# Optimization experiments

Hardware: AMD Instinct MI355X
Metric: run time of the kernel (lower is better)

## Reference

```python
import jax, jax.numpy as jnp
import numpy as np

N_NODES, N_EDGES = 10000, 100000
NODE_DIM, NUM_BASIS = 128, 20
MULS = {0: 128, 1: 64, 2: 32}            # 128x0e + 64x1e + 32x2e
NUM_IRREPS = 224                          # total multiplicity count
HIDDEN = NODE_DIM + NUM_IRREPS            # 352
SPH_DIM = 128 * 1 + 64 * 3 + 32 * 5       # 480
LN_EPS = 1e-5

def _s2_basis():
    # orthonormal (Frobenius) basis of symmetric traceless 3x3 matrices (real l=2)
    s = np.zeros((5, 3, 3)); r2 = 1.0 / np.sqrt(2.0)
    s[0, 0, 1] = s[0, 1, 0] = r2
    s[1, 1, 2] = s[1, 2, 1] = r2
    s[2] = np.diag([-1.0, -1.0, 2.0]) / np.sqrt(6.0)
    s[3, 0, 2] = s[3, 2, 0] = r2
    s[4] = np.diag([1.0, -1.0, 0.0]) * r2
    return s

def _cg_tables():
    # real Clebsch-Gordan tensors for l<=2 built from the invariant tensors
    # delta, Levi-Civita, and the symmetric-traceless basis; unit Frobenius norm (e3nn w3j convention)
    e3 = np.zeros((3, 3, 3))
    e3[0, 1, 2] = e3[1, 2, 0] = e3[2, 0, 1] = 1.0
    e3[0, 2, 1] = e3[2, 1, 0] = e3[1, 0, 2] = -1.0
    S = _s2_basis(); I3 = np.eye(3); I5 = np.eye(5)
    nrm = lambda c: (c / np.linalg.norm(c)).astype(np.float32)
    cg = {(0, 0, 0): np.ones((1, 1, 1), np.float32)}
    cg[(0, 1, 1)] = nrm(I3[None]); cg[(1, 0, 1)] = nrm(I3[:, None, :]); cg[(1, 1, 0)] = nrm(I3[:, :, None])
    cg[(0, 2, 2)] = nrm(I5[None]); cg[(2, 0, 2)] = nrm(I5[:, None, :]); cg[(2, 2, 0)] = nrm(I5[:, :, None])
    cg[(1, 1, 1)] = nrm(e3)
    cg[(1, 1, 2)] = nrm(np.transpose(S, (1, 2, 0)))
    cg[(1, 2, 1)] = nrm(np.transpose(S, (1, 0, 2)))
    cg[(2, 1, 1)] = nrm(S)
    cg[(2, 2, 1)] = nrm(np.einsum('ijk,Mil,Nlj->MNk', e3, S, S))
    cg[(1, 2, 2)] = nrm(np.einsum('iab,Mac,Ncb->iMN', e3, S, S))
    cg[(2, 1, 2)] = nrm(np.einsum('jab,Mac,Ncb->MjN', e3, S, S))
    cg[(2, 2, 2)] = nrm(np.einsum('Mab,Nbc,Pca->MNP', S, S, S))
    return cg

CG = _cg_tables()
PATHS = [(0, 0, 0), (1, 1, 0), (2, 2, 0),
         (0, 1, 1), (1, 0, 1), (1, 1, 1), (1, 2, 1), (2, 1, 1), (2, 2, 1),
         (0, 2, 2), (1, 1, 2), (1, 2, 2), (2, 0, 2), (2, 1, 2), (2, 2, 2)]
FAN = {0: 224, 1: 384, 2: 352}   # e3nn 'element' path-norm fan-in per output irrep
TP_NUMW = sum(MULS[l1] * MULS[l3] for (l1, _, l3) in PATHS)

def _layernorm(x, w, b):
    mu = x.mean(-1, keepdims=True)
    var = ((x - mu) ** 2).mean(-1, keepdims=True)
    return (x - mu) * jax.lax.rsqrt(var + LN_EPS) * w + b

def _o3_layernorm(x, w, b):
    # equivariant layer norm: per-irrep RMS over (mul, m); mean-centering + bias only for scalars
    n = x.shape[0]; outs = []; off = 0; woff = 0
    for l in (0, 1, 2):
        mul, d = MULS[l], 2 * l + 1
        f = x[:, off:off + mul * d].reshape(n, mul, d)
        if l == 0:
            f = f - f.mean(axis=1, keepdims=True)
        nrm = (f * f).mean(axis=(1, 2), keepdims=True)
        f = f * jax.lax.rsqrt(nrm + LN_EPS) * w[woff:woff + mul][None, :, None]
        if l == 0:
            f = f + b[None, :, None]
        outs.append(f.reshape(n, mul * d)); off += mul * d; woff += mul
    return jnp.concatenate(outs, -1)

def _fc_tp(x1, x2, tp_w):
    # FullyConnectedTensorProduct(128x0e+64x1e+32x2e, 1x0e+1x1e+1x2e -> 128x0e+64x1e+32x2e)
    outs = {0: 0.0, 1: 0.0, 2: 0.0}; off = 0
    for (l1, l2, l3) in PATHS:
        m1, m3 = MULS[l1], MULS[l3]
        W = tp_w[off:off + m1 * m3].reshape(m1, m3); off += m1 * m3
        pw = float(np.sqrt((2 * l3 + 1) / FAN[l3]))
        outs[l3] = outs[l3] + pw * jnp.einsum('eum,en,mnk,uw->ewk', x1[l1], x2[l2], jnp.asarray(CG[(l1, l2, l3)]), W, optimize=True)
    e = x2[0].shape[0]
    return jnp.concatenate([outs[l].reshape(e, -1) for l in (0, 1, 2)], -1)

def _forward(x_scalar, x_spherical, rbf, rsh, ln_w, ln_b, o3_w, o3_b,
             mlp_w1, mlp_b1, mlp_w2, mlp_b2, rbf_w, tp_w, edge_index):
    scalar_in = _layernorm(x_scalar, ln_w, ln_b)                # [N,128]
    spherical_in = _o3_layernorm(x_spherical, o3_w, o3_b)       # [N,480]
    h = jax.nn.silu(scalar_in @ mlp_w1 + mlp_b1)
    scalar_out = h @ mlp_w2 + mlp_b2                            # [N,352]
    filt = rbf @ rbf_w                                          # [E,352]
    dst, src = edge_index[0], edge_index[1]
    fo = scalar_out[src] * filt                                 # gather + RBF filter
    gate, msg_scalar = fo[:, :NUM_IRREPS], fo[:, NUM_IRREPS:]
    sph = spherical_in[src]                                     # [E,480]
    e = sph.shape[0]
    # ElementwiseTensorProduct(edge_irreps, 224x0e): per-channel scalar gating
    x1 = {0: (sph[:, :128] * gate[:, :128])[:, :, None],
          1: sph[:, 128:320].reshape(e, 64, 3) * gate[:, 128:192, None],
          2: sph[:, 320:480].reshape(e, 32, 5) * gate[:, 192:224, None]}
    x2 = {0: rsh[:, :1], 1: rsh[:, 1:4], 2: rsh[:, 4:9]}
    msg_sph = _fc_tp(x1, x2, tp_w)                              # [E,480]
    new_scalar = scalar_in.at[dst].add(msg_scalar)
    new_spherical = spherical_in.at[dst].add(msg_sph)
    return new_scalar, new_spherical

def setup_inputs():
    key = jax.random.key(0)
    ks = jax.random.split(key, 9)
    return {
        'x_scalar': jax.random.normal(ks[0], (N_NODES, NODE_DIM), jnp.float32),
        'x_spherical': jax.random.normal(ks[1], (N_NODES, SPH_DIM), jnp.float32),
        'rbf': jax.random.uniform(ks[2], (N_EDGES, NUM_BASIS), jnp.float32),
        'rsh': jax.random.normal(ks[3], (N_EDGES, 9), jnp.float32),
        'edge_index': jax.random.randint(ks[4], (2, N_EDGES), 0, N_NODES, dtype=jnp.int32),
        'ln_w': jnp.ones((NODE_DIM,), jnp.float32),
        'ln_b': jnp.zeros((NODE_DIM,), jnp.float32),
        'o3_w': jnp.ones((NUM_IRREPS,), jnp.float32),
        'o3_b': jnp.zeros((128,), jnp.float32),
        'mlp_w1': jax.random.normal(ks[5], (NODE_DIM, NODE_DIM), jnp.float32) / np.sqrt(NODE_DIM),
        'mlp_b1': jnp.zeros((NODE_DIM,), jnp.float32),
        'mlp_w2': jax.random.normal(ks[6], (NODE_DIM, HIDDEN), jnp.float32) / np.sqrt(NODE_DIM),
        'mlp_b2': jnp.zeros((HIDDEN,), jnp.float32),
        'rbf_w': jax.random.normal(ks[7], (NUM_BASIS, HIDDEN), jnp.float32) / np.sqrt(NUM_BASIS),
        'tp_w': jax.random.normal(ks[8], (TP_NUMW,), jnp.float32),
    }

def reference(x_scalar, x_spherical, rbf, rsh, edge_index, ln_w, ln_b, o3_w, o3_b,
              mlp_w1, mlp_b1, mlp_w2, mlp_b2, rbf_w, tp_w):
    return _forward(x_scalar, x_spherical, rbf, rsh, ln_w, ln_b, o3_w, o3_b,
                    mlp_w1, mlp_b1, mlp_w2, mlp_b2, rbf_w, tp_w, edge_index)
```

## Files before the change

kernel.cpp:

```cpp
#include <hip/hip_runtime.h>

#define NN 10000
#define NE 100000
#define ND 128
#define NB 20
#define NIR 224
#define NH 352
#define SD 480
#define BS 512

#define CR   0.70710678118654752f
#define CA   0.40824829046386302f
#define HA   0.20412414523193151f
#define HR   0.35355339059327376f
#define C110 0.57735026918962576f
#define C220 0.44721359549995794f
#define C111 0.40824829046386302f
#define C11X 0.44721359549995794f
#define C221 0.36514837167011074f
#define C222 0.58554004376912270f
#define S32  0.86602540378443865f
#define PW0  0.066815310478106094f
#define PW1  0.088388347648318447f
#define PW2  0.11918321088232916f

typedef __bf16 v8bf __attribute__((ext_vector_type(8)));
typedef unsigned short us8v __attribute__((ext_vector_type(8)));
typedef float f32x4 __attribute__((ext_vector_type(4)));

__device__ __forceinline__ unsigned short f2bfc(float f) {
  __bf16 h = (__bf16)f;
  return __builtin_bit_cast(unsigned short, h);
}
__device__ __forceinline__ float bf2f(unsigned short h) {
  unsigned int u = ((unsigned int)h) << 16;
  return __builtin_bit_cast(float, u);
}

__device__ __forceinline__ float warpReduceSum(float v) {
  #pragma unroll
  for (int off = 32; off > 0; off >>= 1) v += __shfl_down(v, off, 64);
  return v;
}

__device__ __forceinline__ int t2tT(int t) {
  if (t < 128) return t;
  if (t < 320) { int c = t - 128; return 128 + (c % 3) * 64 + c / 3; }
  int c = t - 320; return 320 + (c % 5) * 32 + c / 5;
}

__global__ __launch_bounds__(256) void sort_hist(const int* __restrict__ ei, int* __restrict__ cnt) {
  int e = blockIdx.x * 256 + threadIdx.x;
  if (e < NE) atomicAdd(&cnt[ei[e]], 1);
}

__global__ __launch_bounds__(1024) void sort_scan(const int* __restrict__ cnt, int* __restrict__ cursor) {
  __shared__ int part[1024];
  const int t = threadIdx.x;
  int loc[10]; int s = 0;
  #pragma unroll
  for (int j = 0; j < 10; ++j) { int idx = t * 10 + j; int v = (idx < NN) ? cnt[idx] : 0; loc[j] = s; s += v; }
  part[t] = s; __syncthreads();
  for (int d = 1; d < 1024; d <<= 1) {
    int v = (t >= d) ? part[t - d] : 0; __syncthreads();
    part[t] += v; __syncthreads();
  }
  int off = part[t] - s;
  #pragma unroll
  for (int j = 0; j < 10; ++j) { int idx = t * 10 + j; if (idx < NN) cursor[idx] = off + loc[j]; }
}

__global__ __launch_bounds__(256) void sort_scatter(
    const int* __restrict__ ei, int* __restrict__ cursor,
    int* __restrict__ es_eid) {
  int e = blockIdx.x * 256 + threadIdx.x;
  if (e < NE) {
    int d = ei[e];
    int pos = atomicAdd(&cursor[d], 1);
    es_eid[pos] = e;
  }
}

__global__ __launch_bounds__(128) void node_ln_kernel(
    const float* __restrict__ xs, const float* __restrict__ xsph,
    const float* __restrict__ lnw, const float* __restrict__ lnb,
    const float* __restrict__ o3w, const float* __restrict__ o3b,
    float* __restrict__ s_in, float* __restrict__ sphT,
    float* __restrict__ out0)
{
  const int n = blockIdx.x, t = threadIdx.x;
  __shared__ float red[4];

  auto reduce2 = [&](float a, float b) {
    a = warpReduceSum(a); b = warpReduceSum(b);
    if ((t & 63) == 0) { red[(t >> 6) * 2] = a; red[(t >> 6) * 2 + 1] = b; }
    __syncthreads();
    float ra = red[0] + red[2], rb = red[1] + red[3];
    __syncthreads();
    return make_float2(ra, rb);
  };

  float x = xs[n * ND + t];
  float2 sr = reduce2(x, x * x);
  float mu = sr.x * (1.f / ND);
  float var = sr.y * (1.f / ND) - mu * mu;
  float y = (x - mu) * rsqrtf(var + 1e-5f) * lnw[t] + lnb[t];
  s_in[n * ND + t] = y; out0[n * ND + t] = y;

  float f = xsph[n * SD + t];
  float2 r0 = reduce2(f, f * f);
  float m0 = r0.x * (1.f / 128.f);
  float nrm0 = r0.y * (1.f / 128.f) - m0 * m0;
  float y0 = (f - m0) * rsqrtf(nrm0 + 1e-5f) * o3w[t] + o3b[t];
  sphT[n * SD + t] = y0;

  float f1a = xsph[n * SD + 128 + t];
  float f1b = (t < 64) ? xsph[n * SD + 256 + t] : 0.f;
  float2 r1 = reduce2(f1a * f1a + f1b * f1b, 0.f);
  float rs1 = rsqrtf(r1.x * (1.f / 192.f) + 1e-5f);
  sphT[n * SD + t2tT(128 + t)] = f1a * rs1 * o3w[128 + t / 3];
  if (t < 64)
    sphT[n * SD + t2tT(256 + t)] = f1b * rs1 * o3w[128 + (128 + t) / 3];

  float f2a = xsph[n * SD + 320 + t];
  float f2b = (t < 32) ? xsph[n * SD + 448 + t] : 0.f;
  float2 r2 = reduce2(f2a * f2a + f2b * f2b, 0.f);
  float rs2 = rsqrtf(r2.x * (1.f / 160.f) + 1e-5f);
  sphT[n * SD + t2tT(320 + t)] = f2a * rs2 * o3w[192 + t / 5];
  if (t < 32)
    sphT[n * SD + t2tT(448 + t)] = f2b * rs2 * o3w[192 + (128 + t) / 5];
}

#define NPB 8
__global__ __launch_bounds__(256) void mlp_kernel(
    const float* __restrict__ s_in, const float* __restrict__ w1,
    const float* __restrict__ b1, const float* __restrict__ w2,
    const float* __restrict__ b2, float* __restrict__ s_out)
{
  __shared__ float sIn[NPB][ND];
  __shared__ float sH[NPB][ND];
  const int t = threadIdx.x;
  const int n0 = blockIdx.x * NPB;
  for (int i = t; i < NPB * ND; i += 256) sIn[i >> 7][i & 127] = s_in[n0 * ND + i];
  __syncthreads();
  {
    const int j = t & 127, g = t >> 7;
    float acc[4] = {0.f, 0.f, 0.f, 0.f};
    for (int k = 0; k < ND; ++k) {
      float w = w1[k * ND + j];
      #pragma unroll
      for (int i = 0; i < 4; ++i) acc[i] = fmaf(sIn[g + 2 * i][k], w, acc[i]);
    }
    #pragma unroll
    for (int i = 0; i < 4; ++i) {
      float z = acc[i] + b1[j];
      sH[g + 2 * i][j] = z / (1.f + __expf(-z));
    }
  }
  __syncthreads();
  for (int jb = 0; jb < 2; ++jb) {
    int j = jb * 256 + t;
    if (j < NH) {
      float acc[NPB];
      #pragma unroll
      for (int i = 0; i < NPB; ++i) acc[i] = b2[j];
      for (int k = 0; k < ND; ++k) {
        float w = w2[k * NH + j];
        #pragma unroll
        for (int i = 0; i < NPB; ++i) acc[i] = fmaf(sH[i][k], w, acc[i]);
      }
      #pragma unroll
      for (int i = 0; i < NPB; ++i) s_out[(n0 + i) * NH + j] = acc[i];
    }
  }
}

__device__ __forceinline__ float wc0(const float* w, int u, int j) {
  int off = (u < 128) ? u * 128 : (u < 192) ? 16384 + (u - 128) * 128 : 24576 + (u - 192) * 128;
  return w[off + j];
}
__device__ __forceinline__ float wc1(const float* w, int u, int j) {
  int off = (u < 128) ? 28672 + u * 64 : (u < 192) ? 36864 + (u - 128) * 64
          : (u < 256) ? 40960 + (u - 192) * 64 : (u < 320) ? 45056 + (u - 256) * 64
          : (u < 352) ? 49152 + (u - 320) * 64 : 51200 + (u - 352) * 64;
  return w[off + j];
}
__device__ __forceinline__ float wc2(const float* w, int u, int j) {
  int off = (u < 128) ? 53248 + u * 32 : (u < 192) ? 57344 + (u - 128) * 32
          : (u < 256) ? 59392 + (u - 192) * 32 : (u < 288) ? 61440 + (u - 256) * 32
          : (u < 320) ? 62464 + (u - 288) * 32 : 63488 + (u - 320) * 32;
  return w[off + j];
}

__global__ __launch_bounds__(256) void prep_w_kernel(
    const float* __restrict__ tpw, const float* __restrict__ rbf_w,
    unsigned short* __restrict__ W0g, unsigned short* __restrict__ W1g,
    unsigned short* __restrict__ W2g, unsigned short* __restrict__ Wfq)
{
  int gid = blockIdx.x * 256 + threadIdx.x;
  int i = gid & 7, lane = (gid >> 3) & 63;
  int r = lane & 15, kl = lane >> 4;
  if (gid < 28672) {
    int fid = gid >> 9, kk = fid >> 3, wid = fid & 7;
    W0g[gid] = f2bfc(wc0(tpw, kk * 32 + kl * 8 + i, wid * 16 + r));
  } else if (gid < 53248) {
    int g = gid - 28672, fid = g >> 9, kk = fid >> 2, nt = fid & 3;
    W1g[g] = f2bfc(wc1(tpw, kk * 32 + kl * 8 + i, nt * 16 + r));
  } else if (gid < 65536) {
    int g = gid - 53248, fid = g >> 9, q = fid >> 2, kh = (fid >> 1) & 1, ntc = fid & 1;
    int kk = kh * 6 + q;
    W2g[g] = (kk < 11) ? f2bfc(wc2(tpw, kk * 32 + kl * 8 + i, ntc * 16 + r)) : (unsigned short)0;
  } else if (gid < 90112) {
    int g = gid - 65536, fid = g >> 9, q = fid >> 3, wid = fid & 7;
    int t44 = wid + q * 8, nt = t44 >> 1, k = kl * 8 + i;
    Wfq[g] = (t44 < 44 && k < 20) ? f2bfc(rbf_w[k * NH + nt * 16 + r]) : (unsigned short)0;
  }
}

template<int M>
__device__ __forceinline__ void emit_dot(unsigned short* dst, const unsigned short* x1,
                                         const int* offs, const float* cf) {
  us8v xv[M];
  #pragma unroll
  for (int m = 0; m < M; ++m) xv[m] = *(const us8v*)&x1[offs[m]];
  v8bf o;
  #pragma unroll
  for (int i = 0; i < 8; ++i) {
    float a = 0.f;
    #pragma unroll
    for (int m = 0; m < M; ++m) a = fmaf(cf[m], bf2f(xv[m][i]), a);
    o[i] = (__bf16)a;
  }
  *(us8v*)dst = __builtin_bit_cast(us8v, o);
}

#define TSW(e, idx) ((idx) ^ (((e) & 7) << 3))

__device__ __forceinline__ void build0(unsigned short* Tb, const unsigned short* X1u,
                                       const float* RshF, int tid) {
  for (int it = tid; it < 32 * 28; it += BS) {
    int e = it / 28, ub = it - e * 28, u0 = ub * 8;
    const float* R = &RshF[e * 9];
    const unsigned short* x1 = &X1u[e * 480];
    unsigned short* dst = Tb + TSW(e, e * 384 + u0);
    if (u0 < 128) {
      float cf[1] = { PW0 * R[0] };
      int offs[1] = { u0 };
      emit_dot<1>(dst, x1, offs, cf);
    } else if (u0 < 192) {
      int m0 = u0 - 128;
      float cf[3] = { PW0 * C110 * R[1], PW0 * C110 * R[2], PW0 * C110 * R[3] };
      int offs[3] = { 128 + m0, 192 + m0, 256 + m0 };
      emit_dot<3>(dst, x1, offs, cf);
    } else {
      int m0 = u0 - 192;
      float cf[5] = { PW0 * C220 * R[4], PW0 * C220 * R[5], PW0 * C220 * R[6],
                      PW0 * C220 * R[7], PW0 * C220 * R[8] };
      int offs[5] = { 320 + m0, 352 + m0, 384 + m0, 416 + m0, 448 + m0 };
      emit_dot<5>(dst, x1, offs, cf);
    }
  }
}

template<int k>
__device__ __forceinline__ void build1(unsigned short* Tb, const unsigned short* X1u,
                                       const float* RshF, int tid) {
  for (int it = tid; it < 32 * 48; it += BS) {
    int e = it / 48, ub = it - e * 48, u0 = ub * 8;
    const float* R = &RshF[e * 9];
    const unsigned short* x1 = &X1u[e * 480];
    unsigned short* dst = Tb + TSW(e, e * 384 + u0);
    const float s = R[0], v0 = R[1], v1 = R[2], v2 = R[3];
    const float w0 = R[4], w1 = R[5], w2 = R[6], w3 = R[7], w4 = R[8];
    if (u0 < 128) {
      float cf[1] = { PW1 * C110 * R[1 + k] };
      int offs[1] = { u0 };
      emit_dot<1>(dst, x1, offs, cf);
    } else if (u0 < 192) {
      float cf[1] = { PW1 * C110 * s };
      int offs[1] = { 128 + k * 64 + (u0 - 128) };
      emit_dot<1>(dst, x1, offs, cf);
    } else if (u0 < 256) {
      constexpr int ka = (k + 1) % 3, kb = (k + 2) % 3;
      int m0 = u0 - 192;
      float cf[2] = { PW1 * C111 * R[1 + kb], -PW1 * C111 * R[1 + ka] };
      int offs[2] = { 128 + ka * 64 + m0, 128 + kb * 64 + m0 };
      emit_dot<2>(dst, x1, offs, cf);
    } else if (u0 < 320) {
      int m0 = u0 - 256;
      float cf[3];
      if constexpr (k == 0) { cf[0] = PW1*C11X*(-CA*w2 + CR*w4); cf[1] = PW1*C11X*CR*w0; cf[2] = PW1*C11X*CR*w3; }
      else if constexpr (k == 1) { cf[0] = PW1*C11X*CR*w0; cf[1] = PW1*C11X*(-CA*w2 - CR*w4); cf[2] = PW1*C11X*CR*w1; }
      else { cf[0] = PW1*C11X*CR*w3; cf[1] = PW1*C11X*CR*w1; cf[2] = PW1*C11X*2.f*CA*w2; }
      int offs[3] = { 128 + m0, 192 + m0, 256 + m0 };
      emit_dot<3>(dst, x1, offs, cf);
    } else if (u0 < 352) {
      int m0 = u0 - 320;
      if constexpr (k == 0) {
        float cf[4] = { PW1*C11X*CR*v1, PW1*C11X*(-CA*v0), PW1*C11X*CR*v2, PW1*C11X*CR*v0 };
        int offs[4] = { 320 + m0, 384 + m0, 416 + m0, 448 + m0 };
        emit_dot<4>(dst, x1, offs, cf);
      } else if constexpr (k == 1) {
        float cf[4] = { PW1*C11X*CR*v0, PW1*C11X*CR*v2, PW1*C11X*(-CA*v1), PW1*C11X*(-CR*v1) };
        int offs[4] = { 320 + m0, 352 + m0, 384 + m0, 448 + m0 };
        emit_dot<4>(dst, x1, offs, cf);
      } else {
        float cf[3] = { PW1*C11X*CR*v1, PW1*C11X*2.f*CA*v2, PW1*C11X*CR*v0 };
        int offs[3] = { 352 + m0, 384 + m0, 416 + m0 };
        emit_dot<3>(dst, x1, offs, cf);
      }
    } else {
      int m0 = u0 - 352;
      if constexpr (k == 0) {
        float cf[5] = { PW1*C221*0.5f*w3, PW1*C221*(S32*w2 + 0.5f*w4), PW1*C221*(-S32*w1),
                        PW1*C221*(-0.5f*w0), PW1*C221*(-0.5f*w1) };
        int offs[5] = { 320 + m0, 352 + m0, 384 + m0, 416 + m0, 448 + m0 };
        emit_dot<5>(dst, x1, offs, cf);
      } else if constexpr (k == 1) {
        float cf[5] = { PW1*C221*(-0.5f*w1), PW1*C221*0.5f*w0, PW1*C221*S32*w3,
                        PW1*C221*(-S32*w2 + 0.5f*w4), PW1*C221*(-0.5f*w3) };
        int offs[5] = { 320 + m0, 352 + m0, 384 + m0, 416 + m0, 448 + m0 };
        emit_dot<5>(dst, x1, offs, cf);
      } else {
        float cf[4] = { PW1*C221*(-w4), PW1*C221*(-0.5f*w3), PW1*C221*0.5f*w1, PW1*C221*w0 };
        int offs[4] = { 320 + m0, 352 + m0, 416 + m0, 448 + m0 };
        emit_dot<4>(dst, x1, offs, cf);
      }
    }
  }
}

template<int K>
__device__ __forceinline__ void build2(unsigned short* Tb, const unsigned short* X1u,
                                       const float* RshF, int tid) {
  for (int it = tid; it < 32 * 44; it += BS) {
    int e = it / 44, ub = it - e * 44, u0 = ub * 8;
    const float* R = &RshF[e * 9];
    const unsigned short* x1 = &X1u[e * 480];
    unsigned short* dst = Tb + TSW(e, e * 384 + u0);
    const float s = R[0], v0 = R[1], v1 = R[2], v2 = R[3];
    const float w0 = R[4], w1 = R[5], w2 = R[6], w3 = R[7], w4 = R[8];
    if (u0 < 128) {
      float cf[1] = { PW2 * C220 * R[4 + K] };
      int offs[1] = { u0 };
      emit_dot<1>(dst, x1, offs, cf);
    } else if (u0 < 192) {
      int m0 = u0 - 128;
      if constexpr (K == 0) {
        float cf[2] = { PW2*C11X*CR*v1, PW2*C11X*CR*v0 };
        int offs[2] = { 128 + m0, 192 + m0 };
        emit_dot<2>(dst, x1, offs, cf);
      } else if constexpr (K == 1) {
        float cf[2] = { PW2*C11X*CR*v2, PW2*C11X*CR*v1 };
        int offs[2] = { 192 + m0, 256 + m0 };
        emit_dot<2>(dst, x1, offs, cf);
      } else if constexpr (K == 2) {
        float cf[3] = { PW2*C11X*(-CA*v0), PW2*C11X*(-CA*v1), PW2*C11X*2.f*CA*v2 };
        int offs[3] = { 128 + m0, 192 + m0, 256 + m0 };
        emit_dot<3>(dst, x1, offs, cf);
      } else if constexpr (K == 3) {
        float cf[2] = { PW2*C11X*CR*v2, PW2*C11X*CR*v0 };
        int offs[2] = { 128 + m0, 256 + m0 };
        emit_dot<2>(dst, x1, offs, cf);
      } else {
        float cf[2] = { PW2*C11X*CR*v0, PW2*C11X*(-CR*v1) };
        int offs[2] = { 128 + m0, 192 + m0 };
        emit_dot<2>(dst, x1, offs, cf);
      }
    } else if (u0 < 256) {
      int m0 = u0 - 192;
      if constexpr (K == 2) {
        float cf[2] = { PW2*C221*S32*w1, PW2*C221*(-S32*w3) };
        int offs[2] = { 128 + m0, 192 + m0 };
        emit_dot<2>(dst, x1, offs, cf);
      } else {
        float cf[3];
        if constexpr (K == 0) { cf[0]=PW2*C221*(-0.5f*w3); cf[1]=PW2*C221*0.5f*w1; cf[2]=PW2*C221*w4; }
        else if constexpr (K == 1) { cf[0]=PW2*C221*(-S32*w2 - 0.5f*w4); cf[1]=PW2*C221*(-0.5f*w0); cf[2]=PW2*C221*0.5f*w3; }
        else if constexpr (K == 3) { cf[0]=PW2*C221*0.5f*w0; cf[1]=PW2*C221*(S32*w2 - 0.5f*w4); cf[2]=PW2*C221*(-0.5f*w1); }
        else { cf[0]=PW2*C221*0.5f*w1; cf[1]=PW2*C221*0.5f*w3; cf[2]=PW2*C221*(-w0); }
        int offs[3] = { 128 + m0, 192 + m0, 256 + m0 };
        emit_dot<3>(dst, x1, offs, cf);
      }
    } else if (u0 < 288) {
      int m0 = u0 - 256;
      float cf[1] = { PW2 * C220 * s };
      int offs[1] = { 320 + K * 32 + m0 };
      emit_dot<1>(dst, x1, offs, cf);
    } else if (u0 < 320) {
      int m0 = u0 - 288;
      if constexpr (K == 0) {
        float cf[3] = { PW2*C221*0.5f*v1, PW2*C221*(-0.5f*v0), PW2*C221*v2 };
        int offs[3] = { 352 + m0, 416 + m0, 448 + m0 };
        emit_dot<3>(dst, x1, offs, cf);
      } else if constexpr (K == 1) {
        float cf[4] = { PW2*C221*(-0.5f*v1), PW2*C221*(-S32*v0), PW2*C221*0.5f*v2, PW2*C221*(-0.5f*v0) };
        int offs[4] = { 320 + m0, 384 + m0, 416 + m0, 448 + m0 };
        emit_dot<4>(dst, x1, offs, cf);
      } else if constexpr (K == 2) {
        float cf[2] = { PW2*C221*S32*v0, PW2*C221*(-S32*v1) };
        int offs[2] = { 352 + m0, 416 + m0 };
        emit_dot<2>(dst, x1, offs, cf);
      } else if constexpr (K == 3) {
        float cf[4] = { PW2*C221*0.5f*v0, PW2*C221*(-0.5f*v2), PW2*C221*S32*v1, PW2*C221*(-0.5f*v1) };
        int offs[4] = { 320 + m0, 352 + m0, 384 + m0, 448 + m0 };
        emit_dot<4>(dst, x1, offs, cf);
      } else {
        float cf[3] = { PW2*C221*(-v2), PW2*C221*0.5f*v0, PW2*C221*0.5f*v1 };
        int offs[3] = { 320 + m0, 352 + m0, 416 + m0 };
        emit_dot<3>(dst, x1, offs, cf);
      }
    } else {
      int m0 = u0 - 320;
      if constexpr (K == 0) {
        float cf[4] = { PW2*C222*(-CA*w2), PW2*C222*HR*w3, PW2*C222*(-CA*w0), PW2*C222*HR*w1 };
        int offs[4] = { 320 + m0, 352 + m0, 384 + m0, 416 + m0 };
        emit_dot<4>(dst, x1, offs, cf);
      } else if constexpr (K == 4) {
        float cf[4] = { PW2*C222*(-HR*w1), PW2*C222*(-CA*w4), PW2*C222*HR*w3, PW2*C222*(-CA*w2) };
        int offs[4] = { 352 + m0, 384 + m0, 416 + m0, 448 + m0 };
        emit_dot<4>(dst, x1, offs, cf);
      } else {
        float cf[5];
        if constexpr (K == 1) { cf[0]=PW2*C222*HR*w3; cf[1]=PW2*C222*(HA*w2 - HR*w4); cf[2]=PW2*C222*HA*w1; cf[3]=PW2*C222*HR*w0; cf[4]=PW2*C222*(-HR*w1); }
        else if constexpr (K == 2) { cf[0]=PW2*C222*(-CA*w0); cf[1]=PW2*C222*HA*w1; cf[2]=PW2*C222*CA*w2; cf[3]=PW2*C222*HA*w3; cf[4]=PW2*C222*(-CA*w4); }
        else { cf[0]=PW2*C222*HR*w1; cf[1]=PW2*C222*HR*w0; cf[2]=PW2*C222*HA*w3; cf[3]=PW2*C222*(HA*w2 + HR*w4); cf[4]=PW2*C222*HR*w3; }
        int offs[5] = { 320 + m0, 352 + m0, 384 + m0, 416 + m0, 448 + m0 };
        emit_dot<5>(dst, x1, offs, cf);
      }
    }
  }
}

__global__ __launch_bounds__(BS, 4) void tp_fused_kernel(
    const float* __restrict__ rbf, const float* __restrict__ rsh,
    const int* __restrict__ ei, const float* __restrict__ s_out,
    const float* __restrict__ sphT,
    const unsigned short* __restrict__ W0g, const unsigned short* __restrict__ W1g,
    const unsigned short* __restrict__ W2g, const unsigned short* __restrict__ Wfq,
    float* __restrict__ out0, unsigned short* __restrict__ msgT)
{
  __shared__ __align__(16) unsigned char smem[81280];
  unsigned short* Tb0 = (unsigned short*)smem;
  unsigned short* Tb1 = (unsigned short*)(smem + 24576);
  unsigned short* gateU = (unsigned short*)smem;
  unsigned short* rbfpadU = (unsigned short*)(smem + 24576);
  unsigned short* X1u = (unsigned short*)(smem + 49152);
  float* RshF = (float*)(smem + 79872);
  int* EdstS = (int*)(smem + 81024);
  int* EsrcS = (int*)(smem + 81152);

  const int tid = threadIdx.x;
  const int wid = tid >> 6, lane = tid & 63;
  const int r = lane & 15, kl = lane >> 4;

  auto MFMA = [](v8bf a, v8bf b, f32x4 c) {
    return __builtin_amdgcn_mfma_f32_16x16x32_bf16(a, b, c, 0, 0, 0);
  };
  auto ldw = [&](const unsigned short* base, int fid) {
    return __builtin_bit_cast(v8bf, *(const us8v*)&base[fid * 512 + lane * 8]);
  };

  auto mfma_l0 = [&](const unsigned short* T, long ebase) {
    f32x4 acc0 = {0.f, 0.f, 0.f, 0.f}, acc1 = {0.f, 0.f, 0.f, 0.f};
    #pragma unroll
    for (int kk = 0; kk < 7; ++kk) {
      v8bf b = ldw(W0g, kk * 8 + wid);
      us8v a0 = *(const us8v*)&T[TSW(r, r * 384 + kl * 8 + kk * 32)];
      us8v a1 = *(const us8v*)&T[TSW(r, (16 + r) * 384 + kl * 8 + kk * 32)];
      acc0 = MFMA(__builtin_bit_cast(v8bf, a0), b, acc0);
      acc1 = MFMA(__builtin_bit_cast(v8bf, a1), b, acc1);
    }
    int col = wid * 16 + r;
    #pragma unroll
    for (int j = 0; j < 4; ++j) {
      msgT[(ebase + kl * 4 + j) * SD + col] = f2bfc(acc0[j]);
      msgT[(ebase + 16 + kl * 4 + j) * SD + col] = f2bfc(acc1[j]);
    }
  };

  auto mfma_l1 = [&](const unsigned short* T, int k, long ebase) {
    const int mt = wid >> 2, nt = wid & 3;
    f32x4 acc = {0.f, 0.f, 0.f, 0.f};
    #pragma unroll
    for (int kk = 0; kk < 12; ++kk) {
      v8bf b = ldw(W1g, kk * 4 + nt);
      us8v a = *(const us8v*)&T[TSW(r, (mt * 16 + r) * 384 + kl * 8 + kk * 32)];
      acc = MFMA(__builtin_bit_cast(v8bf, a), b, acc);
    }
    int col = 128 + k * 64 + nt * 16 + r;
    #pragma unroll
    for (int j = 0; j < 4; ++j)
      msgT[(ebase + mt * 16 + kl * 4 + j) * SD + col] = f2bfc(acc[j]);
  };

  auto mfma_l2 = [&](const unsigned short* T, int K, long ebase) {
    if (wid < 4) {
      const int mt = (wid >> 1) & 1, ntc = wid & 1;
      f32x4 acc = {0.f, 0.f, 0.f, 0.f};
      #pragma unroll
      for (int kk = 0; kk < 11; ++kk) {
        v8bf b = ldw(W2g, (kk % 6) * 4 + (kk / 6) * 2 + ntc);
        us8v a = *(const us8v*)&T[TSW(r, (mt * 16 + r) * 384 + kk * 32 + kl * 8)];
        acc = MFMA(__builtin_bit_cast(v8bf, a), b, acc);
      }
      int col = 320 + K * 32 + ntc * 16 + r;
      #pragma unroll
      for (int j = 0; j < 4; ++j)
        msgT[(ebase + mt * 16 + kl * 4 + j) * SD + col] = f2bfc(acc[j]);
    }
  };

  for (int tile = blockIdx.x; tile < NE / 32; tile += gridDim.x) {
    const int e0 = tile * 32;
    const long ebase = e0;
    for (int i = tid; i < 32; i += BS) { EdstS[i] = ei[e0 + i]; EsrcS[i] = ei[NE + e0 + i]; }
    for (int i = tid; i < 288; i += BS) RshF[i] = rsh[(long)e0 * 9 + i];
    for (int i = tid; i < 1024; i += BS) {
      int e = i >> 5, b = i & 31;
      rbfpadU[e * 40 + b] = (b < 20) ? f2bfc(rbf[(long)(e0 + e) * NB + b]) : (unsigned short)0;
    }
    __syncthreads();
    {
      us8v ra0 = *(const us8v*)&rbfpadU[r * 40 + kl * 8];
      us8v ra1 = *(const us8v*)&rbfpadU[(16 + r) * 40 + kl * 8];
      v8bf av0 = __builtin_bit_cast(v8bf, ra0);
      v8bf av1 = __builtin_bit_cast(v8bf, ra1);
      #pragma unroll
      for (int q = 0; q < 6; ++q) {
        int t44 = wid + q * 8;
        if (t44 < 44) {
          int mt = t44 & 1, nt = t44 >> 1;
          v8bf b = ldw(Wfq, q * 8 + wid);
          f32x4 acc = {0.f, 0.f, 0.f, 0.f};
          acc = MFMA(mt ? av1 : av0, b, acc);
          int gi = nt * 16 + r;
          #pragma unroll
          for (int j = 0; j < 4; ++j) {
            int e = mt * 16 + kl * 4 + j;
            float so = s_out[(long)EsrcS[e] * NH + gi];
            float val = acc[j] * so;
            if (nt < 14) gateU[e * 232 + gi] = f2bfc(val);
            else unsafeAtomicAdd(&out0[(long)EdstS[e] * ND + (gi - 224)], val);
          }
        }
      }
    }
    __syncthreads();
    for (int it = tid; it < 1920; it += BS) {
      int e = it / 60, cb = it - e * 60, c0 = cb * 8;
      long srow = (long)EsrcS[e] * SD;
      int gidx = (c0 < 128) ? c0 : (c0 < 320) ? 128 + (c0 & 63) : 192 + (c0 & 31);
      us8v gv = *(const us8v*)&gateU[e * 232 + gidx];
      const float4 sa = *(const float4*)&sphT[srow + c0];
      const float4 sb = *(const float4*)&sphT[srow + c0 + 4];
      float sv[8] = {sa.x, sa.y, sa.z, sa.w, sb.x, sb.y, sb.z, sb.w};
      v8bf o;
      #pragma unroll
      for (int i = 0; i < 8; ++i) o[i] = (__bf16)(sv[i] * bf2f(gv[i]));
      *(us8v*)&X1u[e * 480 + c0] = __builtin_bit_cast(us8v, o);
    }
    __syncthreads();
    build0(Tb0, X1u, RshF, tid); __syncthreads();
    build1<0>(Tb1, X1u, RshF, tid); mfma_l0(Tb0, ebase); __syncthreads();
    build1<1>(Tb0, X1u, RshF, tid); mfma_l1(Tb1, 0, ebase); __syncthreads();
    build1<2>(Tb1, X1u, RshF, tid); mfma_l1(Tb0, 1, ebase); __syncthreads();
    build2<0>(Tb0, X1u, RshF, tid); mfma_l1(Tb1, 2, ebase); __syncthreads();
    build2<1>(Tb1, X1u, RshF, tid); mfma_l2(Tb0, 0, ebase); __syncthreads();
    build2<2>(Tb0, X1u, RshF, tid); mfma_l2(Tb1, 1, ebase); __syncthreads();
    build2<3>(Tb1, X1u, RshF, tid); mfma_l2(Tb0, 2, ebase); __syncthreads();
    build2<4>(Tb0, X1u, RshF, tid); mfma_l2(Tb1, 3, ebase); __syncthreads();
    mfma_l2(Tb0, 4, ebase); __syncthreads();
  }
}

__global__ __launch_bounds__(512) void gather_kernel(
    const float* __restrict__ sphT, const unsigned short* __restrict__ msgT,
    const int* __restrict__ cnt, const int* __restrict__ cursor,
    const int* __restrict__ es_eid, float* __restrict__ out1)
{
  __shared__ int eids[128];
  __shared__ int s_start, s_deg;
  const int n = blockIdx.x, t = threadIdx.x;
  if (t == 0) {
    int end = cursor[n], d = cnt[n];
    s_start = end - d;
    s_deg = (d > 128) ? 128 : d;
  }
  __syncthreads();
  for (int i = t; i < s_deg; i += 512) eids[i] = es_eid[s_start + i];
  __syncthreads();
  if (t < SD) {
    int tT = t2tT(t);
    float sum = sphT[(long)n * SD + tT];
    for (int i = 0; i < s_deg; ++i)
      sum += bf2f(msgT[(long)eids[i] * SD + tT]);
    out1[(long)n * SD + t] = sum;
  }
}

extern "C" void kernel_launch(void* const* d_in, const int* in_sizes, int n_in,
                              void* d_out, int out_size, void* d_ws, size_t ws_size,
                              hipStream_t stream)
{
  const float* xs   = (const float*)d_in[0];
  const float* xsph = (const float*)d_in[1];
  const float* rbf  = (const float*)d_in[2];
  const float* rsh  = (const float*)d_in[3];
  const int*   ei   = (const int*)d_in[4];
  const float* lnw  = (const float*)d_in[5];
  const float* lnb  = (const float*)d_in[6];
  const float* o3w  = (const float*)d_in[7];
  const float* o3b  = (const float*)d_in[8];
  const float* w1   = (const float*)d_in[9];
  const float* b1   = (const float*)d_in[10];
  const float* w2   = (const float*)d_in[11];
  const float* b2   = (const float*)d_in[12];
  const float* rbfw = (const float*)d_in[13];
  const float* tpw  = (const float*)d_in[14];

  float* out0 = (float*)d_out;
  float* out1 = out0 + (size_t)NN * ND;

  float* ws      = (float*)d_ws;
  float* s_in    = ws;
  float* sphT    = ws + (size_t)NN * ND;
  float* s_out   = ws + (size_t)NN * (ND + SD);
  unsigned short* msgT = (unsigned short*)(ws + (size_t)NN * (ND + SD + NH));
  unsigned short* wbase = msgT + (size_t)NE * SD;
  unsigned short* W0g = wbase;
  unsigned short* W1g = wbase + 28672;
  unsigned short* W2g = wbase + 53248;
  unsigned short* Wfq = wbase + 65536;
  int* ibase  = (int*)(wbase + 90112);
  int* cnt    = ibase;
  int* cursor = ibase + 10000;
  int* es_eid = ibase + 20000;

  hipMemsetAsync(cnt, 0, (size_t)NN * sizeof(int), stream);
  sort_hist<<<(NE + 255) / 256, 256, 0, stream>>>(ei, cnt);
  sort_scan<<<1, 1024, 0, stream>>>(cnt, cursor);
  sort_scatter<<<(NE + 255) / 256, 256, 0, stream>>>(ei, cursor, es_eid);
  prep_w_kernel<<<352, 256, 0, stream>>>(tpw, rbfw, W0g, W1g, W2g, Wfq);
  node_ln_kernel<<<NN, 128, 0, stream>>>(xs, xsph, lnw, lnb, o3w, o3b, s_in, sphT, out0);
  mlp_kernel<<<NN / NPB, 256, 0, stream>>>(s_in, w1, b1, w2, b2, s_out);
  tp_fused_kernel<<<512, BS, 0, stream>>>(rbf, rsh, ei, s_out, sphT,
                                          W0g, W1g, W2g, Wfq, out0, msgT);
  gather_kernel<<<NN, 512, 0, stream>>>(sphT, msgT, cnt, cursor, es_eid, out1);
}
```

Before: 699.2 us.

## Halve edge tile to 16 to double occupancy of fused tensor-product kernel

Shrinks the per-block edge tile in the fused tensor-product kernel from 32 to 16 edges. This halves shared memory use, raises the launch bound to 8 blocks per SM and doubles the grid, and reworks the MFMA wave assignment and the rbf-weight prep layout to match. The aim is more resident blocks to hide latency, at the cost of fewer active waves in the l1/l2 MFMA stages, more tiles and more barriers. The gather kernel now accumulates coalesced along msgT columns into shared memory and permutes afterward, and raises the degree cap from 128 to 160.

```diff
diff --git a/kernel.cpp b/kernel.cpp
--- a/kernel.cpp
+++ b/kernel.cpp
@@ -8,6 +8,8 @@
 #define NH 352
 #define SD 480
 #define BS 512
+#define ET 16
+#define NTILES (NE / ET)
 
 #define CR   0.70710678118654752f
 #define CA   0.40824829046386302f
@@ -71,8 +73,7 @@
 }
 
 __global__ __launch_bounds__(256) void sort_scatter(
-    const int* __restrict__ ei, int* __restrict__ cursor,
-    int* __restrict__ es_eid) {
+    const int* __restrict__ ei, int* __restrict__ cursor, int* __restrict__ es_eid) {
   int e = blockIdx.x * 256 + threadIdx.x;
   if (e < NE) {
     int d = ei[e];
@@ -210,10 +211,10 @@
     int g = gid - 53248, fid = g >> 9, q = fid >> 2, kh = (fid >> 1) & 1, ntc = fid & 1;
     int kk = kh * 6 + q;
     W2g[g] = (kk < 11) ? f2bfc(wc2(tpw, kk * 32 + kl * 8 + i, ntc * 16 + r)) : (unsigned short)0;
-  } else if (gid < 90112) {
+  } else if (gid < 77824) {
     int g = gid - 65536, fid = g >> 9, q = fid >> 3, wid = fid & 7;
-    int t44 = wid + q * 8, nt = t44 >> 1, k = kl * 8 + i;
-    Wfq[g] = (t44 < 44 && k < 20) ? f2bfc(rbf_w[k * NH + nt * 16 + r]) : (unsigned short)0;
+    int t22 = wid + q * 8, k = kl * 8 + i;
+    Wfq[g] = (t22 < 22 && k < 20) ? f2bfc(rbf_w[k * NH + t22 * 16 + r]) : (unsigned short)0;
   }
 }
 
@@ -238,7 +239,7 @@
 
 __device__ __forceinline__ void build0(unsigned short* Tb, const unsigned short* X1u,
                                        const float* RshF, int tid) {
-  for (int it = tid; it < 32 * 28; it += BS) {
+  for (int it = tid; it < ET * 28; it += BS) {
     int e = it / 28, ub = it - e * 28, u0 = ub * 8;
     const float* R = &RshF[e * 9];
     const unsigned short* x1 = &X1u[e * 480];
@@ -265,7 +266,7 @@
 template<int k>
 __device__ __forceinline__ void build1(unsigned short* Tb, const unsigned short* X1u,
                                        const float* RshF, int tid) {
-  for (int it = tid; it < 32 * 48; it += BS) {
+  for (int it = tid; it < ET * 48; it += BS) {
     int e = it / 48, ub = it - e * 48, u0 = ub * 8;
     const float* R = &RshF[e * 9];
     const unsigned short* x1 = &X1u[e * 480];
@@ -333,7 +334,7 @@
 template<int K>
 __device__ __forceinline__ void build2(unsigned short* Tb, const unsigned short* X1u,
                                        const float* RshF, int tid) {
-  for (int it = tid; it < 32 * 44; it += BS) {
+  for (int it = tid; it < ET * 44; it += BS) {
     int e = it / 44, ub = it - e * 44, u0 = ub * 8;
     const float* R = &RshF[e * 9];
     const unsigned short* x1 = &X1u[e * 480];
@@ -432,7 +433,7 @@
   }
 }
 
-__global__ __launch_bounds__(BS, 4) void tp_fused_kernel(
+__global__ __launch_bounds__(BS, 8) void tp_fused_kernel(
     const float* __restrict__ rbf, const float* __restrict__ rsh,
     const int* __restrict__ ei, const float* __restrict__ s_out,
     const float* __restrict__ sphT,
@@ -440,15 +441,15 @@
     const unsigned short* __restrict__ W2g, const unsigned short* __restrict__ Wfq,
     float* __restrict__ out0, unsigned short* __restrict__ msgT)
 {
-  __shared__ __align__(16) unsigned char smem[81280];
+  __shared__ __align__(16) unsigned char smem[40640];
   unsigned short* Tb0 = (unsigned short*)smem;
-  unsigned short* Tb1 = (unsigned short*)(smem + 24576);
+  unsigned short* Tb1 = (unsigned short*)(smem + 12288);
   unsigned short* gateU = (unsigned short*)smem;
-  unsigned short* rbfpadU = (unsigned short*)(smem + 24576);
-  unsigned short* X1u = (unsigned short*)(smem + 49152);
-  float* RshF = (float*)(smem + 79872);
-  int* EdstS = (int*)(smem + 81024);
-  int* EsrcS = (int*)(smem + 81152);
+  unsigned short* rbfpadU = (unsigned short*)(smem + 12288);
+  unsigned short* X1u = (unsigned short*)(smem + 24576);
+  float* RshF = (float*)(smem + 39936);
+  int* EdstS = (int*)(smem + 40512);
+  int* EsrcS = (int*)(smem + 40576);
 
   const int tid = threadIdx.x;
   const int wid = tid >> 6, lane = tid & 63;
@@ -462,92 +463,87 @@
   };
 
   auto mfma_l0 = [&](const unsigned short* T, long ebase) {
-    f32x4 acc0 = {0.f, 0.f, 0.f, 0.f}, acc1 = {0.f, 0.f, 0.f, 0.f};
+    f32x4 acc = {0.f, 0.f, 0.f, 0.f};
     #pragma unroll
     for (int kk = 0; kk < 7; ++kk) {
       v8bf b = ldw(W0g, kk * 8 + wid);
-      us8v a0 = *(const us8v*)&T[TSW(r, r * 384 + kl * 8 + kk * 32)];
-      us8v a1 = *(const us8v*)&T[TSW(r, (16 + r) * 384 + kl * 8 + kk * 32)];
-      acc0 = MFMA(__builtin_bit_cast(v8bf, a0), b, acc0);
-      acc1 = MFMA(__builtin_bit_cast(v8bf, a1), b, acc1);
+      us8v a = *(const us8v*)&T[TSW(r, r * 384 + kl * 8 + kk * 32)];
+      acc = MFMA(__builtin_bit_cast(v8bf, a), b, acc);
     }
     int col = wid * 16 + r;
     #pragma unroll
-    for (int j = 0; j < 4; ++j) {
-      msgT[(ebase + kl * 4 + j) * SD + col] = f2bfc(acc0[j]);
-      msgT[(ebase + 16 + kl * 4 + j) * SD + col] = f2bfc(acc1[j]);
-    }
+    for (int j = 0; j < 4; ++j)
+      msgT[(ebase + kl * 4 + j) * SD + col] = f2bfc(acc[j]);
   };
 
   auto mfma_l1 = [&](const unsigned short* T, int k, long ebase) {
-    const int mt = wid >> 2, nt = wid & 3;
-    f32x4 acc = {0.f, 0.f, 0.f, 0.f};
-    #pragma unroll
-    for (int kk = 0; kk < 12; ++kk) {
-      v8bf b = ldw(W1g, kk * 4 + nt);
-      us8v a = *(const us8v*)&T[TSW(r, (mt * 16 + r) * 384 + kl * 8 + kk * 32)];
-      acc = MFMA(__builtin_bit_cast(v8bf, a), b, acc);
-    }
-    int col = 128 + k * 64 + nt * 16 + r;
-    #pragma unroll
-    for (int j = 0; j < 4; ++j)
-      msgT[(ebase + mt * 16 + kl * 4 + j) * SD + col] = f2bfc(acc[j]);
+    if (wid < 4) {
+      const int nt = wid;
+      f32x4 acc = {0.f, 0.f, 0.f, 0.f};
+      #pragma unroll
+      for (int kk = 0; kk < 12; ++kk) {
+        v8bf b = ldw(W1g, kk * 4 + nt);
+        us8v a = *(const us8v*)&T[TSW(r, r * 384 + kl * 8 + kk * 32)];
+        acc = MFMA(__builtin_bit_cast(v8bf, a), b, acc);
+      }
+      int col = 128 + k * 64 + nt * 16 + r;
+      #pragma unroll
+      for (int j = 0; j < 4; ++j)
+        msgT[(ebase + kl * 4 + j) * SD + col] = f2bfc(acc[j]);
+    }
   };
 
   auto mfma_l2 = [&](const unsigned short* T, int K, long ebase) {
-    if (wid < 4) {
-      const int mt = (wid >> 1) & 1, ntc = wid & 1;
+    if (wid < 2) {
+      const int ntc = wid;
       f32x4 acc = {0.f, 0.f, 0.f, 0.f};
       #pragma unroll
       for (int kk = 0; kk < 11; ++kk) {
         v8bf b = ldw(W2g, (kk % 6) * 4 + (kk / 6) * 2 + ntc);
-        us8v a = *(const us8v*)&T[TSW(r, (mt * 16 + r) * 384 + kk * 32 + kl * 8)];
+        us8v a = *(const us8v*)&T[TSW(r, r * 384 + kk * 32 + kl * 8)];
         acc = MFMA(__builtin_bit_cast(v8bf, a), b, acc);
       }
       int col = 320 + K * 32 + ntc * 16 + r;
       #pragma unroll
       for (int j = 0; j < 4; ++j)
-        msgT[(ebase + mt * 16 + kl * 4 + j) * SD + col] = f2bfc(acc[j]);
+        msgT[(ebase + kl * 4 + j) * SD + col] = f2bfc(acc[j]);
     }
   };
 
-  for (int tile = blockIdx.x; tile < NE / 32; tile += gridDim.x) {
-    const int e0 = tile * 32;
+  for (int tile = blockIdx.x; tile < NTILES; tile += gridDim.x) {
+    const int e0 = tile * ET;
     const long ebase = e0;
-    for (int i = tid; i < 32; i += BS) { EdstS[i] = ei[e0 + i]; EsrcS[i] = ei[NE + e0 + i]; }
-    for (int i = tid; i < 288; i += BS) RshF[i] = rsh[(long)e0 * 9 + i];
-    for (int i = tid; i < 1024; i += BS) {
+    for (int i = tid; i < ET; i += BS) { EdstS[i] = ei[e0 + i]; EsrcS[i] = ei[NE + e0 + i]; }
+    for (int i = tid; i < ET * 9; i += BS) RshF[i] = rsh[(long)e0 * 9 + i];
+    for (int i = tid; i < ET * 32; i += BS) {
       int e = i >> 5, b = i & 31;
       rbfpadU[e * 40 + b] = (b < 20) ? f2bfc(rbf[(long)(e0 + e) * NB + b]) : (unsigned short)0;
     }
     __syncthreads();
     {
-      us8v ra0 = *(const us8v*)&rbfpadU[r * 40 + kl * 8];
-      us8v ra1 = *(const us8v*)&rbfpadU[(16 + r) * 40 + kl * 8];
-      v8bf av0 = __builtin_bit_cast(v8bf, ra0);
-      v8bf av1 = __builtin_bit_cast(v8bf, ra1);
-      #pragma unroll
-      for (int q = 0; q < 6; ++q) {
-        int t44 = wid + q * 8;
-        if (t44 < 44) {
-          int mt = t44 & 1, nt = t44 >> 1;
+      us8v ra = *(const us8v*)&rbfpadU[r * 40 + kl * 8];
+      v8bf av = __builtin_bit_cast(v8bf, ra);
+      #pragma unroll
+      for (int q = 0; q < 3; ++q) {
+        int t22 = wid + q * 8;
+        if (t22 < 22) {
           v8bf b = ldw(Wfq, q * 8 + wid);
           f32x4 acc = {0.f, 0.f, 0.f, 0.f};
-          acc = MFMA(mt ? av1 : av0, b, acc);
-          int gi = nt * 16 + r;
+          acc = MFMA(av, b, acc);
+          int gi = t22 * 16 + r;
           #pragma unroll
           for (int j = 0; j < 4; ++j) {
-            int e = mt * 16 + kl * 4 + j;
+            int e = kl * 4 + j;
             float so = s_out[(long)EsrcS[e] * NH + gi];
             float val = acc[j] * so;
-            if (nt < 14) gateU[e * 232 + gi] = f2bfc(val);
+            if (t22 < 14) gateU[e * 232 + gi] = f2bfc(val);
             else unsafeAtomicAdd(&out0[(long)EdstS[e] * ND + (gi - 224)], val);
           }
         }
       }
     }
     __syncthreads();
-    for (int it = tid; it < 1920; it += BS) {
+    for (int it = tid; it < ET * 60; it += BS) {
       int e = it / 60, cb = it - e * 60, c0 = cb * 8;
       long srow = (long)EsrcS[e] * SD;
       int gidx = (c0 < 128) ? c0 : (c0 < 320) ? 128 + (c0 & 63) : 192 + (c0 & 31);
@@ -579,23 +575,29 @@
     const int* __restrict__ cnt, const int* __restrict__ cursor,
     const int* __restrict__ es_eid, float* __restrict__ out1)
 {
-  __shared__ int eids[128];
-  __shared__ int s_start, s_deg;
+  __shared__ float sumT[SD];
+  __shared__ int eids[160];
+  __shared__ int s_deg;
   const int n = blockIdx.x, t = threadIdx.x;
   if (t == 0) {
-    int end = cursor[n], d = cnt[n];
-    s_start = end - d;
-    s_deg = (d > 128) ? 128 : d;
+    int d = cnt[n];
+    s_deg = (d > 160) ? 160 : d;
   }
   __syncthreads();
-  for (int i = t; i < s_deg; i += 512) eids[i] = es_eid[s_start + i];
+  int deg = s_deg;
+  int start = cursor[n] - cnt[n];
+  for (int i = t; i < deg; i += 512) eids[i] = es_eid[start + i];
+  __syncthreads();
+  if (t < SD) {
+    float acc = 0.f;
+    for (int i = 0; i < deg; ++i)
+      acc += bf2f(msgT[(long)eids[i] * SD + t]);
+    sumT[t] = acc;
+  }
   __syncthreads();
   if (t < SD) {
     int tT = t2tT(t);
-    float sum = sphT[(long)n * SD + tT];
-    for (int i = 0; i < s_deg; ++i)
-      sum += bf2f(msgT[(long)eids[i] * SD + tT]);
-    out1[(long)n * SD + t] = sum;
+    out1[(long)n * SD + t] = sphT[(long)n * SD + tT] + sumT[tT];
   }
 }
 
@@ -632,7 +634,7 @@
   unsigned short* W1g = wbase + 28672;
   unsigned short* W2g = wbase + 53248;
   unsigned short* Wfq = wbase + 65536;
-  int* ibase  = (int*)(wbase + 90112);
+  int* ibase  = (int*)(wbase + 77824);
   int* cnt    = ibase;
   int* cursor = ibase + 10000;
   int* es_eid = ibase + 20000;
@@ -641,10 +643,10 @@
   sort_hist<<<(NE + 255) / 256, 256, 0, stream>>>(ei, cnt);
   sort_scan<<<1, 1024, 0, stream>>>(cnt, cursor);
   sort_scatter<<<(NE + 255) / 256, 256, 0, stream>>>(ei, cursor, es_eid);
-  prep_w_kernel<<<352, 256, 0, stream>>>(tpw, rbfw, W0g, W1g, W2g, Wfq);
+  prep_w_kernel<<<304, 256, 0, stream>>>(tpw, rbfw, W0g, W1g, W2g, Wfq);
   node_ln_kernel<<<NN, 128, 0, stream>>>(xs, xsph, lnw, lnb, o3w, o3b, s_in, sphT, out0);
   mlp_kernel<<<NN / NPB, 256, 0, stream>>>(s_in, w1, b1, w2, b2, s_out);
-  tp_fused_kernel<<<512, BS, 0, stream>>>(rbf, rsh, ei, s_out, sphT,
-                                          W0g, W1g, W2g, Wfq, out0, msgT);
+  tp_fused_kernel<<<1024, BS, 0, stream>>>(rbf, rsh, ei, s_out, sphT,
+                                           W0g, W1g, W2g, Wfq, out0, msgT);
   gather_kernel<<<NN, 512, 0, stream>>>(sphT, msgT, cnt, cursor, es_eid, out1);
 }
```

Measured after the change: 658.7 us. -5.8%, faster.
